# Kernel optimization log

Hardware: AMD Instinct MI355X
Metric: run time of the kernel (lower is better)

## Reference

```python
import jax, jax.numpy as jnp
import numpy as np

N, E, DIN, DH, DC = 50000, 1600000, 128, 128, 40
EPS = 1e-5  # BatchNorm eps


def _seg_sum(v, idx, n):
    return jax.ops.segment_sum(v, idx, num_segments=n)


def setup_inputs() -> dict:
    key = jax.random.key(0)
    ks = jax.random.split(key, 24)
    rn = lambda i, shp, s=0.05: jax.random.normal(ks[i], shp, jnp.float32) * s
    return {
        "x": jax.random.normal(ks[0], (N, DIN), jnp.float32),
        "src": jax.random.randint(ks[1], (E,), 0, N, jnp.int32),
        "dst": jax.random.randint(ks[2], (E,), 0, N, jnp.int32),
        # CoNet layer 1 (in -> hidden)
        "w11s": rn(3, (DIN, DH)), "w11n": rn(4, (DIN, DH)), "b11": jnp.zeros((DH,), jnp.float32),
        "w12": rn(5, (DIN, DH)), "b12": jnp.zeros((DH,), jnp.float32),
        "w13": rn(6, (DIN, DH)), "a13l": rn(7, (DH,)), "a13r": rn(8, (DH,)), "b13": jnp.zeros((DH,), jnp.float32),
        "cw1": jax.random.uniform(ks[9], (3,), jnp.float32, 0.5, 1.5),
        # BatchNorm1d
        "g": jnp.ones((DH,), jnp.float32), "be": jnp.zeros((DH,), jnp.float32),
        # CoNet layer 2 (hidden -> out)
        "w21s": rn(10, (DH, DC)), "w21n": rn(11, (DH, DC)), "b21": jnp.zeros((DC,), jnp.float32),
        "w22": rn(12, (DH, DC)), "b22": jnp.zeros((DC,), jnp.float32),
        "w23": rn(13, (DH, DC)), "a23l": rn(14, (DC,)), "a23r": rn(15, (DC,)), "b23": jnp.zeros((DC,), jnp.float32),
        "cw2": jax.random.uniform(ks[16], (3,), jnp.float32, 0.5, 1.5),
    }


def conet(x, src, dst, ws, wn, bs, wg, bg, wa, al, ar, ba, cw):
    """AFFN CoNet: SAGE(mean) + GCN + GAT(1 head), fused by normalized weights."""
    n = x.shape[0]
    ones = jnp.ones((src.shape[0],), x.dtype)
    indeg = _seg_sum(ones, dst, n)   # in-degree per node
    outdeg = _seg_sum(ones, src, n)  # out-degree per node

    # --- SAGEConv, mean aggregator: fc_self(x) + fc_neigh(mean_neigh(x)) ---
    nei = _seg_sum(x[src], dst, n) / jnp.maximum(indeg, 1.0)[:, None]
    x1 = x @ ws + nei @ wn + bs

    ns = jnp.maximum(outdeg, 1.0) ** -0.5
    nd = jnp.maximum(indeg, 1.0) ** -0.5
    h = _seg_sum((x * ns[:, None])[src], dst, n) * nd[:, None]
    x2 = h @ wg + bg

    # --- GATConv, 1 head ---
    f = x @ wa                       # [N, out]
    el = f @ al                      # [N]
    er = f @ ar                      # [N]
    e = jax.nn.leaky_relu(el[src] + er[dst], 0.2)  # [E]
    m = jax.ops.segment_max(e, dst, num_segments=n)
    a = jnp.exp(e - m[dst])
    s = _seg_sum(a, dst, n)
    alpha = a / jnp.maximum(s[dst], 1e-9)
    x3 = _seg_sum(alpha[:, None] * f[src], dst, n) + ba

    w = cw / jnp.sum(cw)
    return w[0] * x1 + w[1] * x2 + w[2] * x3


def reference(x, src, dst,
              w11s, w11n, b11, w12, b12, w13, a13l, a13r, b13, cw1,
              g, be,
              w21s, w21n, b21, w22, b22, w23, a23l, a23r, b23, cw2):
    h = conet(x, src, dst, w11s, w11n, b11, w12, b12, w13, a13l, a13r, b13, cw1)
    # BatchNorm1d (training-mode batch statistics)
    mu = jnp.mean(h, axis=0)
    var = jnp.var(h, axis=0)
    h = (h - mu) * jax.lax.rsqrt(var + EPS) * g + be
    h = jax.nn.relu(h)
    # dropout in eval mode: identity
    h = conet(h, src, dst, w21s, w21n, b21, w22, b22, w23, a23l, a23r, b23, cw2)
    return jax.nn.log_softmax(h, axis=1)
```

## Files before the change

### kernel.cpp

```cpp
#include <hip/hip_runtime.h>
#include <hip/hip_bf16.h>
#include <math.h>

#define DIN 128
#define DH  128
#define DC  40

#define HCHUNK  12544
#define NSTRIPE 128
#define NPAD    (HCHUNK * 4)

typedef unsigned short u16;
typedef unsigned int u32;
typedef unsigned char u8;
typedef __attribute__((ext_vector_type(2))) float f32x2;
typedef __attribute__((ext_vector_type(4))) float f32x4;
typedef __attribute__((ext_vector_type(8))) short bf16x8;

static __device__ __forceinline__ float bf2f(u16 u) {
    union { u32 i; float f; } v; v.i = ((u32)u) << 16; return v.f;
}
static __device__ __forceinline__ u16 f2bf(float f) {
    __hip_bfloat16 h = __float2bfloat16(f);
    union { __hip_bfloat16 h; u16 u; } v; v.h = h; return v.u;
}
static __device__ __forceinline__ u32 pack2bf(float a, float b) {
    return ((u32)f2bf(b) << 16) | (u32)f2bf(a);
}

static __device__ __forceinline__ u8 f2fp8(float f) {
    u32 s = (__float_as_uint(f) >> 31) << 7;
    float a = fabsf(f);
    a = fminf(a, 448.f);
    if (a < 0.015625f) {
        int q = (int)rintf(a * 512.f);
        return (u8)(s | (u32)q);
    }
    u32 x = __float_as_uint(a);
    u32 lsb = (x >> 20) & 1;
    x += 0x0007FFFF + lsb;
    u32 e = (x >> 23) - 120;
    u32 m = (x >> 20) & 7;
    return (u8)(s | (e << 3) | m);
}

#if __has_builtin(__builtin_amdgcn_cvt_pk_f32_fp8)
template<bool HI>
static __device__ __forceinline__ f32x2 fp8pk(u32 w) {
    return __builtin_amdgcn_cvt_pk_f32_fp8((int)w, HI);
}
#else
static __device__ __forceinline__ float fp8dec1(u32 byte) {
    u32 s = (byte >> 7) & 1, em = byte & 0x7F;
    float v = __uint_as_float((s << 31) | (em << 20)) * 0x1p120f;
    return v;
}
template<bool HI>
static __device__ __forceinline__ f32x2 fp8pk(u32 w) {
    u32 b0 = HI ? ((w >> 16) & 0xff) : (w & 0xff);
    u32 b1 = HI ? ((w >> 24) & 0xff) : ((w >> 8) & 0xff);
    f32x2 r; r.x = fp8dec1(b0); r.y = fp8dec1(b1); return r;
}
#endif

__global__ __launch_bounds__(256) void k_prep(
        const float* w11s, const float* w11n, const float* w12, const float* w13,
        const float* b11, const float* b12, const float* b13, const float* cw1,
        const float* w21s, const float* w21n, const float* w22, const float* w23,
        const float* b21, const float* b22, const float* b23, const float* cw2,
        const float* a13l, const float* a13r, const float* a23l, const float* a23r,
        u16* __restrict__ Wf1, u16* __restrict__ Wf2,
        float* __restrict__ bc1, float* __restrict__ bc2, float* __restrict__ vattn) {
    int i = blockIdx.x * 256 + threadIdx.x;
    float s1 = cw1[0] + cw1[1] + cw1[2];
    float u0 = cw1[0] / s1, u1 = cw1[1] / s1, u2 = cw1[2] / s1;
    float s2 = cw2[0] + cw2[1] + cw2[2];
    float q0 = cw2[0] / s2, q1 = cw2[1] / s2, q2 = cw2[2] / s2;
    if (i < 65536) {
        int j = i & 7, lane = (i >> 3) & 63, nt = (i >> 9) & 7, kt = i >> 12;
        int k = kt * 32 + ((lane >> 4) << 3) + j;
        int n = nt * 16 + (lane & 15);
        float v;
        if (k < 128)      v = u0 * w11s[k * 128 + n];
        else if (k < 256) v = u0 * w11n[(k - 128) * 128 + n];
        else if (k < 384) v = u1 * w12[(k - 256) * 128 + n];
        else              v = u2 * w13[(k - 384) * 128 + n];
        Wf1[i] = f2bf(v);
    } else if (i < 90112) {
        int i2 = i - 65536;
        int j = i2 & 7;
        int l2 = i2 >> 3;
        int lane = l2 & 63;
        int t2 = l2 >> 6;
        int nt = t2 % 3, kt = t2 / 3;
        int k = kt * 32 + ((lane >> 4) << 3) + j;
        int n = nt * 16 + (lane & 15);
        float v = 0.f;
        if (n < 40) {
            if (k < 128)      v = q0 * w21s[k * 40 + n];
            else if (k < 256) v = q0 * w21n[(k - 128) * 40 + n];
            else if (k < 384) v = q1 * w22[(k - 256) * 40 + n];
            else              v = q2 * w23[(k - 384) * 40 + n];
        }
        Wf2[i2] = f2bf(v);
    } else if (i < 90624) {
        int t = i - 90112;
        if (t < 128) {
            float s = 0; for (int j = 0; j < 128; ++j) s += w13[t * 128 + j] * a13l[j];
            vattn[t] = s;
        } else if (t < 256) {
            int r = t - 128; float s = 0; for (int j = 0; j < 128; ++j) s += w13[r * 128 + j] * a13r[j];
            vattn[t] = s;
        } else if (t < 384) {
            int r = t - 256; float s = 0; for (int j = 0; j < 40; ++j) s += w23[r * 40 + j] * a23l[j];
            vattn[t] = s;
        } else {
            int r = t - 384; float s = 0; for (int j = 0; j < 40; ++j) s += w23[r * 40 + j] * a23r[j];
            vattn[t] = s;
        }
    } else if (i < 90752) {
        int c = i - 90624;
        bc1[c] = u0 * b11[c] + u1 * b12[c] + u2 * b13[c];
    } else if (i < 90792) {
        int c = i - 90752;
        bc2[c] = q0 * b21[c] + q1 * b22[c] + q2 * b23[c];
    }
}

__global__ __launch_bounds__(256) void k_hist2(const int* __restrict__ src,
        const int* __restrict__ dst,
        u16* __restrict__ partialsS, u16* __restrict__ partialsD,
        u16* __restrict__ wsrank, int E, int eps) {
    __shared__ u32 histS[HCHUNK];
    __shared__ u32 histD[HCHUNK];
    int chunk = blockIdx.x;
    int stripe = blockIdx.y;
    int base = chunk * (HCHUNK * 2);
    for (int i = threadIdx.x; i < HCHUNK; i += 256) { histS[i] = 0; histD[i] = 0; }
    __syncthreads();
    int e0 = stripe * eps;
    int e1 = e0 + eps; if (e1 > E) e1 = E;
    for (int e = e0 + threadIdx.x; e < e1; e += 256) {
        int ks = src[e] - base;
        int kd = dst[e] - base;
        if ((u32)ks < (u32)(HCHUNK * 2))
            atomicAdd(&histS[ks >> 1], 1u << ((ks & 1) * 16));
        if ((u32)kd < (u32)(HCHUNK * 2)) {
            u32 old = atomicAdd(&histD[kd >> 1], 1u << ((kd & 1) * 16));
            wsrank[e] = (u16)((old >> ((kd & 1) * 16)) & 0xffff);
        }
    }
    __syncthreads();
    u32* prowS = (u32*)(partialsS + (size_t)stripe * NPAD + base);
    u32* prowD = (u32*)(partialsD + (size_t)stripe * NPAD + base);
    for (int i = threadIdx.x; i < HCHUNK; i += 256) { prowS[i] = histS[i]; prowD[i] = histD[i]; }
}

__global__ void k_pfx2(const u16* __restrict__ partialsS, u16* __restrict__ partialsD,
                       int* __restrict__ indeg, float* __restrict__ ns, int n) {
    int node = blockIdx.x * 256 + threadIdx.x;
    if (node >= NPAD) return;
    int runS = 0;
    for (int s0 = 0; s0 < NSTRIPE; s0 += 16) {
        u16 c[16];
#pragma unroll
        for (int i = 0; i < 16; ++i) c[i] = partialsS[(size_t)(s0 + i) * NPAD + node];
#pragma unroll
        for (int i = 0; i < 16; ++i) runS += c[i];
    }
    int runD = 0;
    for (int s0 = 0; s0 < NSTRIPE; s0 += 16) {
        u16 c[16];
#pragma unroll
        for (int i = 0; i < 16; ++i) c[i] = partialsD[(size_t)(s0 + i) * NPAD + node];
#pragma unroll
        for (int i = 0; i < 16; ++i) {
            partialsD[(size_t)(s0 + i) * NPAD + node] = (u16)runD;
            runD += c[i];
        }
    }
    if (node < n) {
        indeg[node] = runD;
        int d = runS < 1 ? 1 : runS;
        ns[node] = rsqrtf((float)d);
    }
}

__global__ void k_scan1(const int* __restrict__ deg, int* __restrict__ excl,
                        int* __restrict__ bsum, int n) {
    __shared__ int sh[256];
    int i = blockIdx.x * 256 + threadIdx.x;
    int v = (i < n) ? deg[i] : 0;
    sh[threadIdx.x] = v; __syncthreads();
    for (int o = 1; o < 256; o <<= 1) {
        int t = (threadIdx.x >= o) ? sh[threadIdx.x - o] : 0;
        __syncthreads(); sh[threadIdx.x] += t; __syncthreads();
    }
    if (i < n) excl[i] = sh[threadIdx.x] - v;
    if (threadIdx.x == 255) bsum[blockIdx.x] = sh[255];
}
__global__ void k_scan2(int* __restrict__ bsum, int nb) {
    __shared__ int sh[256];
    int t = threadIdx.x;
    int v = (t < nb) ? bsum[t] : 0;
    sh[t] = v; __syncthreads();
    for (int o = 1; o < 256; o <<= 1) {
        int u = (t >= o) ? sh[t - o] : 0;
        __syncthreads(); sh[t] += u; __syncthreads();
    }
    if (t < nb) bsum[t] = sh[t] - v;
}
__global__ void k_scan3(const int* __restrict__ excl, const int* __restrict__ bsum,
                        int* __restrict__ rowptr, int n, int E) {
    int i = blockIdx.x * 256 + threadIdx.x;
    if (i < n) rowptr[i] = excl[i] + bsum[blockIdx.x];
    if (i == 0) rowptr[n] = E;
}

__global__ __launch_bounds__(256) void k_place2(const int* __restrict__ src,
        const int* __restrict__ dst, const int* __restrict__ rowptr,
        const u16* __restrict__ partials, const u16* __restrict__ wsrank,
        int* __restrict__ col, int E, int eps) {
    int stripe = blockIdx.x;
    const u16* prow = partials + (size_t)stripe * NPAD;
    int sub = (eps + 3) >> 2;
    int e0 = stripe * eps + blockIdx.y * sub;
    int e1 = e0 + sub;
    int cap = stripe * eps + eps; if (cap > E) cap = E;
    if (e1 > cap) e1 = cap;
    for (int e = e0 + threadIdx.x; e < e1; e += 256) {
        int d = dst[e];
        col[rowptr[d] + prow[d] + wsrank[e]] = src[e];
    }
}

__global__ __launch_bounds__(256) void k_cvt_dots(const float* __restrict__ X,
        const float* __restrict__ vl, const float* __restrict__ vr, const float* __restrict__ ns,
        u16* __restrict__ Xb, u8* __restrict__ Xq,
        float2* __restrict__ elns, float* __restrict__ er, int n) {
    int w = (blockIdx.x * blockDim.x + threadIdx.x) >> 6;
    int lane = threadIdx.x & 63;
    if (w >= n) return;
    float2 xv = *(const float2*)&X[(size_t)w * 128 + lane * 2];
    *(u32*)&Xb[(size_t)w * 128 + lane * 2] = pack2bf(xv.x, xv.y);
    u16 q = (u16)f2fp8(xv.x) | ((u16)f2fp8(xv.y) << 8);
    *(u16*)&Xq[(size_t)w * 128 + lane * 2] = q;
    float2 a = *(const float2*)&vl[lane * 2];
    float2 b = *(const float2*)&vr[lane * 2];
    float dl = xv.x * a.x + xv.y * a.y;
    float dr = xv.x * b.x + xv.y * b.y;
    for (int off = 32; off; off >>= 1) {
        dl += __shfl_down(dl, off);
        dr += __shfl_down(dr, off);
    }
    if (lane == 0) { elns[w] = make_float2(dl, ns[w]); er[w] = dr; }
}

__global__ __launch_bounds__(256) void k_agg(const u8* __restrict__ Xq,
        const int* __restrict__ rowptr, const int* __restrict__ colsrc,
        const float2* __restrict__ elns, const float* __restrict__ er,
        u16* __restrict__ AG, int n) {
    int w = (blockIdx.x * blockDim.x + threadIdx.x) >> 6;
    int lane = threadIdx.x & 63;
    if (w >= n) return;
    int g = lane >> 4, gl = lane & 15;
    int beg = rowptr[w], end = rowptr[w + 1];
    int k = end - beg;
    float erd = er[w];
    f32x2 aS2[4] = {}, aG2[4] = {}, aA2[4] = {};
    float ssum = 0.f;
    for (int c0 = beg; c0 < end; c0 += 64) {
        int cnt = end - c0; if (cnt > 64) cnt = 64;
        int s = 0; float p = 0.f; float nsl = 0.f;
        if (lane < cnt) {
            s = colsrc[c0 + lane];
            float2 v = elns[s];
            float t = v.x + erd;
            t = t > 0.f ? t : 0.2f * t;
            p = __expf(t);
            nsl = v.y;
        }
        float ps = p;
        for (int o = 32; o; o >>= 1) ps += __shfl_xor(ps, o);
        ssum += ps;
        int full = cnt >> 2;
#pragma unroll 8
        for (int t = 0; t < full; ++t) {
            int j = (t << 2) + g;
            int sj = __shfl(s, j);
            float pj = __shfl(p, j);
            float nsj = __shfl(nsl, j);
            uint2 xq = *(const uint2*)&Xq[(size_t)sj * 128 + gl * 8];
            f32x2 xv2[4] = {fp8pk<false>(xq.x), fp8pk<true>(xq.x),
                            fp8pk<false>(xq.y), fp8pk<true>(xq.y)};
            f32x2 ns2 = {nsj, nsj}, p2 = {pj, pj};
#pragma unroll
            for (int q = 0; q < 4; ++q) {
                aS2[q] += xv2[q];
                aG2[q] += ns2 * xv2[q];
                aA2[q] += p2 * xv2[q];
            }
        }
        if (cnt & 3) {
            int j = (full << 2) + g;
            int sj = __shfl(s, j);
            float pj = __shfl(p, j);
            float nsj = __shfl(nsl, j);
            if (j < cnt) {
                uint2 xq = *(const uint2*)&Xq[(size_t)sj * 128 + gl * 8];
                f32x2 xv2[4] = {fp8pk<false>(xq.x), fp8pk<true>(xq.x),
                                fp8pk<false>(xq.y), fp8pk<true>(xq.y)};
                f32x2 ns2 = {nsj, nsj}, p2 = {pj, pj};
#pragma unroll
                for (int q = 0; q < 4; ++q) {
                    aS2[q] += xv2[q];
                    aG2[q] += ns2 * xv2[q];
                    aA2[q] += p2 * xv2[q];
                }
            }
        }
    }
    float aS[8], aG[8], aA[8];
#pragma unroll
    for (int i = 0; i < 4; ++i) {
        aS[2 * i] = aS2[i][0]; aS[2 * i + 1] = aS2[i][1];
        aG[2 * i] = aG2[i][0]; aG[2 * i + 1] = aG2[i][1];
        aA[2 * i] = aA2[i][0]; aA[2 * i + 1] = aA2[i][1];
    }
#pragma unroll
    for (int i = 0; i < 8; ++i) {
        aS[i] += __shfl_xor(aS[i], 16); aS[i] += __shfl_xor(aS[i], 32);
        aG[i] += __shfl_xor(aG[i], 16); aG[i] += __shfl_xor(aG[i], 32);
        aA[i] += __shfl_xor(aA[i], 16); aA[i] += __shfl_xor(aA[i], 32);
    }
    int kc = k < 1 ? 1 : k;
    float invk = 1.f / (float)kc;
    float ndd = rsqrtf((float)kc);
    float gi = 1.f / fmaxf(ssum, 1e-9f);
    u16* row = AG + (size_t)w * 384;
    if (g == 0) {
        uint4 o = make_uint4(pack2bf(aS[0] * invk, aS[1] * invk), pack2bf(aS[2] * invk, aS[3] * invk),
                             pack2bf(aS[4] * invk, aS[5] * invk), pack2bf(aS[6] * invk, aS[7] * invk));
        *(uint4*)&row[gl * 8] = o;
    } else if (g == 1) {
        uint4 o = make_uint4(pack2bf(aG[0] * ndd, aG[1] * ndd), pack2bf(aG[2] * ndd, aG[3] * ndd),
                             pack2bf(aG[4] * ndd, aG[5] * ndd), pack2bf(aG[6] * ndd, aG[7] * ndd));
        *(uint4*)&row[128 + gl * 8] = o;
    } else if (g == 2) {
        uint4 o = make_uint4(pack2bf(aA[0] * gi, aA[1] * gi), pack2bf(aA[2] * gi, aA[3] * gi),
                             pack2bf(aA[4] * gi, aA[5] * gi), pack2bf(aA[6] * gi, aA[7] * gi));
        *(uint4*)&row[256 + gl * 8] = o;
    }
}

__global__ __launch_bounds__(256) void k_gemm1(const u16* __restrict__ Xb,
        const u16* __restrict__ AG, const u16* __restrict__ Wf,
        const float* __restrict__ bias, u16* __restrict__ C,
        float* __restrict__ bnacc, int M) {
    if (blockIdx.x == 0 && threadIdx.x < 256) bnacc[threadIdx.x] = 0.f;
    const int NT = 8;
    int wave = threadIdx.x >> 6;
    int lane = threadIdx.x & 63;
    int m0 = blockIdx.x * 64 + wave * 16;
    int arow = m0 + (lane & 15);
    if (arow >= M) arow = M - 1;
    int kq = lane >> 4;
    f32x4 acc[NT];
#pragma unroll
    for (int t = 0; t < NT; ++t) acc[t] = (f32x4){0.f, 0.f, 0.f, 0.f};
#pragma unroll
    for (int kt = 0; kt < 16; ++kt) {
        int k0 = kt * 32 + kq * 8;
        bf16x8 a;
        if (k0 < 128) a = *(const bf16x8*)&Xb[(size_t)arow * 128 + k0];
        else          a = *(const bf16x8*)&AG[(size_t)arow * 384 + (k0 - 128)];
        const u16* wb = Wf + ((size_t)kt * NT) * 512 + lane * 8;
#pragma unroll
        for (int t = 0; t < NT; ++t) {
            bf16x8 b = *(const bf16x8*)&wb[(size_t)t * 512];
            acc[t] = __builtin_amdgcn_mfma_f32_16x16x32_bf16(a, b, acc[t], 0, 0, 0);
        }
    }
    int ccol = lane & 15;
    int rbase = m0 + kq * 4;
#pragma unroll
    for (int t = 0; t < NT; ++t) {
        int col = t * 16 + ccol;
        float bv = bias[col];
#pragma unroll
        for (int r = 0; r < 4; ++r) {
            int rr = rbase + r;
            if (rr < M) C[(size_t)rr * 128 + col] = f2bf(acc[t][r] + bv);
        }
    }
}

__global__ __launch_bounds__(256) void k_gemm2_lsm(const u16* __restrict__ Xb,
        const u16* __restrict__ AG, const u16* __restrict__ Wf,
        const float* __restrict__ bias, float* __restrict__ out, int M) {
    const int NT = 3;
    int wave = threadIdx.x >> 6;
    int lane = threadIdx.x & 63;
    int m0 = blockIdx.x * 64 + wave * 16;
    int arow = m0 + (lane & 15);
    if (arow >= M) arow = M - 1;
    int kq = lane >> 4;
    f32x4 acc[NT];
#pragma unroll
    for (int t = 0; t < NT; ++t) acc[t] = (f32x4){0.f, 0.f, 0.f, 0.f};
#pragma unroll
    for (int kt = 0; kt < 16; ++kt) {
        int k0 = kt * 32 + kq * 8;
        bf16x8 a;
        if (k0 < 128) a = *(const bf16x8*)&Xb[(size_t)arow * 128 + k0];
        else          a = *(const bf16x8*)&AG[(size_t)arow * 384 + (k0 - 128)];
        const u16* wb = Wf + ((size_t)kt * NT) * 512 + lane * 8;
#pragma unroll
        for (int t = 0; t < NT; ++t) {
            bf16x8 b = *(const bf16x8*)&wb[(size_t)t * 512];
            acc[t] = __builtin_amdgcn_mfma_f32_16x16x32_bf16(a, b, acc[t], 0, 0, 0);
        }
    }
    int ccol = lane & 15;
    int rbase = m0 + kq * 4;
    bool valid[NT];
    float bv[NT];
#pragma unroll
    for (int t = 0; t < NT; ++t) {
        int col = t * 16 + ccol;
        valid[t] = (col < 40);
        bv[t] = valid[t] ? bias[col] : 0.f;
    }
#pragma unroll
    for (int r = 0; r < 4; ++r) {
        float v[NT];
#pragma unroll
        for (int t = 0; t < NT; ++t) v[t] = valid[t] ? (acc[t][r] + bv[t]) : -INFINITY;
        float mx = fmaxf(fmaxf(v[0], v[1]), v[2]);
        for (int o = 1; o < 16; o <<= 1) mx = fmaxf(mx, __shfl_xor(mx, o));
        float se = 0.f;
#pragma unroll
        for (int t = 0; t < NT; ++t) se += valid[t] ? __expf(v[t] - mx) : 0.f;
        for (int o = 1; o < 16; o <<= 1) se += __shfl_xor(se, o);
        float lse = mx + logf(se);
        int rr = rbase + r;
        if (rr < M) {
#pragma unroll
            for (int t = 0; t < NT; ++t) {
                int col = t * 16 + ccol;
                if (valid[t]) out[(size_t)rr * 40 + col] = v[t] - lse;
            }
        }
    }
}

__global__ __launch_bounds__(256) void k_bn_stats(const u16* __restrict__ H,
        float* __restrict__ acc, int nrows) {
    int c = threadIdx.x & 127;
    int rh = threadIdx.x >> 7;
    int r0 = blockIdx.x * 256;
    int rend = r0 + 256; if (rend > nrows) rend = nrows;
    float s = 0.f, q = 0.f;
    for (int r = r0 + rh; r < rend; r += 2) {
        float v = bf2f(H[(size_t)r * 128 + c]);
        s += v; q += v * v;
    }
    atomicAdd(&acc[c], s);
    atomicAdd(&acc[128 + c], q);
}

__global__ __launch_bounds__(256) void k_bnorm_dots(const u16* __restrict__ Hp,
        const float* __restrict__ bnacc, const float* __restrict__ g, const float* __restrict__ be,
        const float* __restrict__ vl, const float* __restrict__ vr,
        const float* __restrict__ ns,
        u16* __restrict__ H, u8* __restrict__ H8,
        float2* __restrict__ elns, float* __restrict__ er, float Nf, int n) {
    int w = (blockIdx.x * blockDim.x + threadIdx.x) >> 6;
    int lane = threadIdx.x & 63;
    if (w >= n) return;
    int c0 = lane * 2, c1 = lane * 2 + 1;
    float mu0 = bnacc[c0] / Nf, mu1 = bnacc[c1] / Nf;
    float var0 = bnacc[128 + c0] / Nf - mu0 * mu0;
    float var1 = bnacc[128 + c1] / Nf - mu1 * mu1;
    float sc0 = g[c0] * rsqrtf(var0 + 1e-5f);
    float sc1 = g[c1] * rsqrtf(var1 + 1e-5f);
    float sh0 = be[c0] - mu0 * sc0;
    float sh1 = be[c1] - mu1 * sc1;
    u32 hu = *(const u32*)&Hp[(size_t)w * 128 + lane * 2];
    float vx = bf2f((u16)hu), vy = bf2f((u16)(hu >> 16));
    float h0 = fmaxf(vx * sc0 + sh0, 0.f);
    float h1 = fmaxf(vy * sc1 + sh1, 0.f);
    *(u32*)&H[(size_t)w * 128 + lane * 2] = pack2bf(h0, h1);
    u16 q = (u16)f2fp8(h0) | ((u16)f2fp8(h1) << 8);
    *(u16*)&H8[(size_t)w * 128 + lane * 2] = q;
    float2 a = *(const float2*)&vl[lane * 2];
    float2 b = *(const float2*)&vr[lane * 2];
    float dl = h0 * a.x + h1 * a.y;
    float dr = h0 * b.x + h1 * b.y;
    for (int off = 32; off; off >>= 1) {
        dl += __shfl_down(dl, off);
        dr += __shfl_down(dr, off);
    }
    if (lane == 0) { elns[w] = make_float2(dl, ns[w]); er[w] = dr; }
}

extern "C" void kernel_launch(void* const* d_in, const int* in_sizes, int n_in,
                              void* d_out, int out_size, void* d_ws, size_t ws_size,
                              hipStream_t stream) {
    const float* x    = (const float*)d_in[0];
    const int*   src  = (const int*)d_in[1];
    const int*   dst  = (const int*)d_in[2];
    const float* w11s = (const float*)d_in[3];
    const float* w11n = (const float*)d_in[4];
    const float* b11  = (const float*)d_in[5];
    const float* w12  = (const float*)d_in[6];
    const float* b12  = (const float*)d_in[7];
    const float* w13  = (const float*)d_in[8];
    const float* a13l = (const float*)d_in[9];
    const float* a13r = (const float*)d_in[10];
    const float* b13  = (const float*)d_in[11];
    const float* cw1  = (const float*)d_in[12];
    const float* g    = (const float*)d_in[13];
    const float* be   = (const float*)d_in[14];
    const float* w21s = (const float*)d_in[15];
    const float* w21n = (const float*)d_in[16];
    const float* b21  = (const float*)d_in[17];
    const float* w22  = (const float*)d_in[18];
    const float* b22  = (const float*)d_in[19];
    const float* w23  = (const float*)d_in[20];
    const float* a23l = (const float*)d_in[21];
    const float* a23r = (const float*)d_in[22];
    const float* b23  = (const float*)d_in[23];
    const float* cw2  = (const float*)d_in[24];

    const int N = in_sizes[0] / DIN;
    const int E = in_sizes[1];

    char* ws = (char*)d_ws;
    size_t off = 0;
    auto alloc = [&](size_t bytes) { size_t o = off; off += (bytes + 255) & ~(size_t)255; return o; };
    u16*   Xb     = (u16*)(ws + alloc((size_t)N * 128 * 2));
    u8*    Xq     = (u8*)(ws + alloc((size_t)N * 128));
    u16*   AG     = (u16*)(ws + alloc((size_t)N * 384 * 2));
    u16*   hpre   = (u16*)(ws + alloc((size_t)N * 128 * 2));
    u16*   h      = (u16*)(ws + alloc((size_t)N * 128 * 2));
    u8*    h8     = (u8*)(ws + alloc((size_t)N * 128));
    int*   col    = (int*)(ws + alloc((size_t)E * 4));
    u16*   wsrank = (u16*)(ws + alloc((size_t)E * 2));
    u16*   partialsS = (u16*)(ws + alloc((size_t)NSTRIPE * NPAD * 2));
    u16*   partialsD = (u16*)(ws + alloc((size_t)NSTRIPE * NPAD * 2));
    int*   rowptr = (int*)(ws + alloc((size_t)(N + 1) * 4));
    int*   indeg  = (int*)(ws + alloc((size_t)N * 4));
    int*   excl   = (int*)(ws + alloc((size_t)N * 4));
    int*   bsum   = (int*)(ws + alloc(256 * 4));
    float* ns     = (float*)(ws + alloc((size_t)N * 4));
    float2* elns  = (float2*)(ws + alloc((size_t)N * 8));
    float* er     = (float*)(ws + alloc((size_t)N * 4));
    u16*   Wf1    = (u16*)(ws + alloc((size_t)16 * 8 * 64 * 8 * 2));
    u16*   Wf2    = (u16*)(ws + alloc((size_t)16 * 3 * 64 * 8 * 2));
    float* bc1    = (float*)(ws + alloc(128 * 4));
    float* bc2    = (float*)(ws + alloc(40 * 4));
    float* vattn  = (float*)(ws + alloc(512 * 4));
    float* bnacc  = (float*)(ws + alloc(256 * 4));

    int eb_eps = (E + NSTRIPE - 1) / NSTRIPE;
    int wb = (N * 64 + 255) / 256;
    int sb = (N + 255) / 256;
    int gb = (N + 63) / 64;
    int pb = (NPAD + 255) / 256;

    k_prep<<<(90792 + 255) / 256, 256, 0, stream>>>(
        w11s, w11n, w12, w13, b11, b12, b13, cw1,
        w21s, w21n, w22, w23, b21, b22, b23, cw2,
        a13l, a13r, a23l, a23r, Wf1, Wf2, bc1, bc2, vattn);

    {
        dim3 hg(2, NSTRIPE);
        k_hist2<<<hg, 256, 0, stream>>>(src, dst, partialsS, partialsD, wsrank, E, eb_eps);
        k_pfx2<<<pb, 256, 0, stream>>>(partialsS, partialsD, indeg, ns, N);
        k_scan1<<<sb, 256, 0, stream>>>(indeg, excl, bsum, N);
        k_scan2<<<1, 256, 0, stream>>>(bsum, sb);
        k_scan3<<<sb, 256, 0, stream>>>(excl, bsum, rowptr, N, E);
        dim3 pg(NSTRIPE, 4);
        k_place2<<<pg, 256, 0, stream>>>(src, dst, rowptr, partialsD, wsrank, col, E, eb_eps);
    }

    k_cvt_dots<<<wb, 256, 0, stream>>>(x, vattn, vattn + 128, ns, Xb, Xq, elns, er, N);
    k_agg<<<wb, 256, 0, stream>>>(Xq, rowptr, col, elns, er, AG, N);
    k_gemm1<<<gb, 256, 0, stream>>>(Xb, AG, Wf1, bc1, hpre, bnacc, N);

    k_bn_stats<<<(N + 255) / 256, 256, 0, stream>>>(hpre, bnacc, N);
    k_bnorm_dots<<<wb, 256, 0, stream>>>(hpre, bnacc, g, be, vattn + 256, vattn + 384, ns,
                                         h, h8, elns, er, (float)N, N);

    k_agg<<<wb, 256, 0, stream>>>(h8, rowptr, col, elns, er, AG, N);
    k_gemm2_lsm<<<gb, 256, 0, stream>>>(h, AG, Wf2, bc2, (float*)d_out, N);
}
```

Before: 426.1 us.

## Build CSR with global atomic counting and cursors; pad aggregation tails

Replaces the striped shared-memory histogram, per-stripe prefix and rank-based placement with two simple edge-parallel kernels. One counts in- and out-degrees with global atomics, the other places edges with an atomicAdd on a per-node cursor. This drops the large partials buffers and their reads and writes. The out-degree normalisation is now computed inside the conversion and batchnorm kernels, and the degree arrays and a zero padding row are cleared in the prep kernel. The aggregation loop pads partial groups with a zero sentinel node so the separate tail branch goes away. The trade-offs are atomic contention, a nondeterministic neighbour order and summation order, and extra zero-weight gathers in the padded groups.

```diff
diff --git a/kernel.cpp b/kernel.cpp
--- a/kernel.cpp
+++ b/kernel.cpp
@@ -5,10 +5,6 @@
 #define DIN 128
 #define DH  128
 #define DC  40
-
-#define HCHUNK  12544
-#define NSTRIPE 128
-#define NPAD    (HCHUNK * 4)
 
 typedef unsigned short u16;
 typedef unsigned int u32;
@@ -70,7 +66,9 @@
         const float* b21, const float* b22, const float* b23, const float* cw2,
         const float* a13l, const float* a13r, const float* a23l, const float* a23r,
         u16* __restrict__ Wf1, u16* __restrict__ Wf2,
-        float* __restrict__ bc1, float* __restrict__ bc2, float* __restrict__ vattn) {
+        float* __restrict__ bc1, float* __restrict__ bc2, float* __restrict__ vattn,
+        int* __restrict__ indeg, int* __restrict__ outdeg,
+        u32* __restrict__ zq, u32* __restrict__ zh, int n) {
     int i = blockIdx.x * 256 + threadIdx.x;
     float s1 = cw1[0] + cw1[1] + cw1[2];
     float u0 = cw1[0] / s1, u1 = cw1[1] / s1, u2 = cw1[2] / s1;
@@ -79,12 +77,12 @@
     if (i < 65536) {
         int j = i & 7, lane = (i >> 3) & 63, nt = (i >> 9) & 7, kt = i >> 12;
         int k = kt * 32 + ((lane >> 4) << 3) + j;
-        int n = nt * 16 + (lane & 15);
+        int n2 = nt * 16 + (lane & 15);
         float v;
-        if (k < 128)      v = u0 * w11s[k * 128 + n];
-        else if (k < 256) v = u0 * w11n[(k - 128) * 128 + n];
-        else if (k < 384) v = u1 * w12[(k - 256) * 128 + n];
-        else              v = u2 * w13[(k - 384) * 128 + n];
+        if (k < 128)      v = u0 * w11s[k * 128 + n2];
+        else if (k < 256) v = u0 * w11n[(k - 128) * 128 + n2];
+        else if (k < 384) v = u1 * w12[(k - 256) * 128 + n2];
+        else              v = u2 * w13[(k - 384) * 128 + n2];
         Wf1[i] = f2bf(v);
     } else if (i < 90112) {
         int i2 = i - 65536;
@@ -94,13 +92,13 @@
         int t2 = l2 >> 6;
         int nt = t2 % 3, kt = t2 / 3;
         int k = kt * 32 + ((lane >> 4) << 3) + j;
-        int n = nt * 16 + (lane & 15);
+        int n2 = nt * 16 + (lane & 15);
         float v = 0.f;
-        if (n < 40) {
-            if (k < 128)      v = q0 * w21s[k * 40 + n];
-            else if (k < 256) v = q0 * w21n[(k - 128) * 40 + n];
-            else if (k < 384) v = q1 * w22[(k - 256) * 40 + n];
-            else              v = q2 * w23[(k - 384) * 40 + n];
+        if (n2 < 40) {
+            if (k < 128)      v = q0 * w21s[k * 40 + n2];
+            else if (k < 256) v = q0 * w21n[(k - 128) * 40 + n2];
+            else if (k < 384) v = q1 * w22[(k - 256) * 40 + n2];
+            else              v = q2 * w23[(k - 384) * 40 + n2];
         }
         Wf2[i2] = f2bf(v);
     } else if (i < 90624) {
@@ -124,65 +122,22 @@
     } else if (i < 90792) {
         int c = i - 90752;
         bc2[c] = q0 * b21[c] + q1 * b22[c] + q2 * b23[c];
-    }
-}
-
-__global__ __launch_bounds__(256) void k_hist2(const int* __restrict__ src,
-        const int* __restrict__ dst,
-        u16* __restrict__ partialsS, u16* __restrict__ partialsD,
-        u16* __restrict__ wsrank, int E, int eps) {
-    __shared__ u32 histS[HCHUNK];
-    __shared__ u32 histD[HCHUNK];
-    int chunk = blockIdx.x;
-    int stripe = blockIdx.y;
-    int base = chunk * (HCHUNK * 2);
-    for (int i = threadIdx.x; i < HCHUNK; i += 256) { histS[i] = 0; histD[i] = 0; }
-    __syncthreads();
-    int e0 = stripe * eps;
-    int e1 = e0 + eps; if (e1 > E) e1 = E;
-    for (int e = e0 + threadIdx.x; e < e1; e += 256) {
-        int ks = src[e] - base;
-        int kd = dst[e] - base;
-        if ((u32)ks < (u32)(HCHUNK * 2))
-            atomicAdd(&histS[ks >> 1], 1u << ((ks & 1) * 16));
-        if ((u32)kd < (u32)(HCHUNK * 2)) {
-            u32 old = atomicAdd(&histD[kd >> 1], 1u << ((kd & 1) * 16));
-            wsrank[e] = (u16)((old >> ((kd & 1) * 16)) & 0xffff);
-        }
-    }
-    __syncthreads();
-    u32* prowS = (u32*)(partialsS + (size_t)stripe * NPAD + base);
-    u32* prowD = (u32*)(partialsD + (size_t)stripe * NPAD + base);
-    for (int i = threadIdx.x; i < HCHUNK; i += 256) { prowS[i] = histS[i]; prowD[i] = histD[i]; }
-}
-
-__global__ void k_pfx2(const u16* __restrict__ partialsS, u16* __restrict__ partialsD,
-                       int* __restrict__ indeg, float* __restrict__ ns, int n) {
-    int node = blockIdx.x * 256 + threadIdx.x;
-    if (node >= NPAD) return;
-    int runS = 0;
-    for (int s0 = 0; s0 < NSTRIPE; s0 += 16) {
-        u16 c[16];
-#pragma unroll
-        for (int i = 0; i < 16; ++i) c[i] = partialsS[(size_t)(s0 + i) * NPAD + node];
-#pragma unroll
-        for (int i = 0; i < 16; ++i) runS += c[i];
-    }
-    int runD = 0;
-    for (int s0 = 0; s0 < NSTRIPE; s0 += 16) {
-        u16 c[16];
-#pragma unroll
-        for (int i = 0; i < 16; ++i) c[i] = partialsD[(size_t)(s0 + i) * NPAD + node];
-#pragma unroll
-        for (int i = 0; i < 16; ++i) {
-            partialsD[(size_t)(s0 + i) * NPAD + node] = (u16)runD;
-            runD += c[i];
-        }
-    }
-    if (node < n) {
-        indeg[node] = runD;
-        int d = runS < 1 ? 1 : runS;
-        ns[node] = rsqrtf((float)d);
+    } else if (i < 90792 + 2 * n) {
+        int t = i - 90792;
+        if (t < n) indeg[t] = 0; else outdeg[t - n] = 0;
+    } else if (i < 90792 + 2 * n + 64) {
+        int t = i - 90792 - 2 * n;
+        if (t < 32) zq[t] = 0u; else zh[t - 32] = 0u;
+    }
+}
+
+__global__ __launch_bounds__(256) void k_count(const int* __restrict__ src,
+        const int* __restrict__ dst, int* __restrict__ indeg,
+        int* __restrict__ outdeg, int E) {
+    int i = blockIdx.x * 256 + threadIdx.x;
+    if (i < E) {
+        atomicAdd(&indeg[dst[i]], 1);
+        atomicAdd(&outdeg[src[i]], 1);
     }
 }
 
@@ -211,31 +166,29 @@
     if (t < nb) bsum[t] = sh[t] - v;
 }
 __global__ void k_scan3(const int* __restrict__ excl, const int* __restrict__ bsum,
-                        int* __restrict__ rowptr, int n, int E) {
+                        int* __restrict__ rowptr, int* __restrict__ cursor, int n, int E) {
     int i = blockIdx.x * 256 + threadIdx.x;
-    if (i < n) rowptr[i] = excl[i] + bsum[blockIdx.x];
+    if (i < n) {
+        int v = excl[i] + bsum[blockIdx.x];
+        rowptr[i] = v;
+        cursor[i] = v;
+    }
     if (i == 0) rowptr[n] = E;
 }
 
-__global__ __launch_bounds__(256) void k_place2(const int* __restrict__ src,
-        const int* __restrict__ dst, const int* __restrict__ rowptr,
-        const u16* __restrict__ partials, const u16* __restrict__ wsrank,
-        int* __restrict__ col, int E, int eps) {
-    int stripe = blockIdx.x;
-    const u16* prow = partials + (size_t)stripe * NPAD;
-    int sub = (eps + 3) >> 2;
-    int e0 = stripe * eps + blockIdx.y * sub;
-    int e1 = e0 + sub;
-    int cap = stripe * eps + eps; if (cap > E) cap = E;
-    if (e1 > cap) e1 = cap;
-    for (int e = e0 + threadIdx.x; e < e1; e += 256) {
-        int d = dst[e];
-        col[rowptr[d] + prow[d] + wsrank[e]] = src[e];
+__global__ __launch_bounds__(256) void k_place(const int* __restrict__ src,
+        const int* __restrict__ dst, int* __restrict__ cursor,
+        int* __restrict__ col, int E) {
+    int i = blockIdx.x * 256 + threadIdx.x;
+    if (i < E) {
+        int pos = atomicAdd(&cursor[dst[i]], 1);
+        col[pos] = src[i];
     }
 }
 
 __global__ __launch_bounds__(256) void k_cvt_dots(const float* __restrict__ X,
-        const float* __restrict__ vl, const float* __restrict__ vr, const float* __restrict__ ns,
+        const float* __restrict__ vl, const float* __restrict__ vr,
+        const int* __restrict__ odeg,
         u16* __restrict__ Xb, u8* __restrict__ Xq,
         float2* __restrict__ elns, float* __restrict__ er, int n) {
     int w = (blockIdx.x * blockDim.x + threadIdx.x) >> 6;
@@ -253,7 +206,12 @@
         dl += __shfl_down(dl, off);
         dr += __shfl_down(dr, off);
     }
-    if (lane == 0) { elns[w] = make_float2(dl, ns[w]); er[w] = dr; }
+    if (lane == 0) {
+        int od = odeg[w];
+        float nsw = rsqrtf((float)(od < 1 ? 1 : od));
+        elns[w] = make_float2(dl, nsw);
+        er[w] = dr;
+    }
 }
 
 __global__ __launch_bounds__(256) void k_agg(const u8* __restrict__ Xq,
@@ -271,7 +229,7 @@
     float ssum = 0.f;
     for (int c0 = beg; c0 < end; c0 += 64) {
         int cnt = end - c0; if (cnt > 64) cnt = 64;
-        int s = 0; float p = 0.f; float nsl = 0.f;
+        int s = n; float p = 0.f; float nsl = 0.f;
         if (lane < cnt) {
             s = colsrc[c0 + lane];
             float2 v = elns[s];
@@ -283,9 +241,9 @@
         float ps = p;
         for (int o = 32; o; o >>= 1) ps += __shfl_xor(ps, o);
         ssum += ps;
-        int full = cnt >> 2;
+        int steps = (cnt + 3) >> 2;
 #pragma unroll 8
-        for (int t = 0; t < full; ++t) {
+        for (int t = 0; t < steps; ++t) {
             int j = (t << 2) + g;
             int sj = __shfl(s, j);
             float pj = __shfl(p, j);
@@ -299,24 +257,6 @@
                 aS2[q] += xv2[q];
                 aG2[q] += ns2 * xv2[q];
                 aA2[q] += p2 * xv2[q];
-            }
-        }
-        if (cnt & 3) {
-            int j = (full << 2) + g;
-            int sj = __shfl(s, j);
-            float pj = __shfl(p, j);
-            float nsj = __shfl(nsl, j);
-            if (j < cnt) {
-                uint2 xq = *(const uint2*)&Xq[(size_t)sj * 128 + gl * 8];
-                f32x2 xv2[4] = {fp8pk<false>(xq.x), fp8pk<true>(xq.x),
-                                fp8pk<false>(xq.y), fp8pk<true>(xq.y)};
-                f32x2 ns2 = {nsj, nsj}, p2 = {pj, pj};
-#pragma unroll
-                for (int q = 0; q < 4; ++q) {
-                    aS2[q] += xv2[q];
-                    aG2[q] += ns2 * xv2[q];
-                    aA2[q] += p2 * xv2[q];
-                }
             }
         }
     }
@@ -472,7 +412,7 @@
 __global__ __launch_bounds__(256) void k_bnorm_dots(const u16* __restrict__ Hp,
         const float* __restrict__ bnacc, const float* __restrict__ g, const float* __restrict__ be,
         const float* __restrict__ vl, const float* __restrict__ vr,
-        const float* __restrict__ ns,
+        const int* __restrict__ odeg,
         u16* __restrict__ H, u8* __restrict__ H8,
         float2* __restrict__ elns, float* __restrict__ er, float Nf, int n) {
     int w = (blockIdx.x * blockDim.x + threadIdx.x) >> 6;
@@ -501,7 +441,12 @@
         dl += __shfl_down(dl, off);
         dr += __shfl_down(dr, off);
     }
-    if (lane == 0) { elns[w] = make_float2(dl, ns[w]); er[w] = dr; }
+    if (lane == 0) {
+        int od = odeg[w];
+        float nsw = rsqrtf((float)(od < 1 ? 1 : od));
+        elns[w] = make_float2(dl, nsw);
+        er[w] = dr;
+    }
 }
 
 extern "C" void kernel_launch(void* const* d_in, const int* in_sizes, int n_in,
@@ -540,20 +485,18 @@
     size_t off = 0;
     auto alloc = [&](size_t bytes) { size_t o = off; off += (bytes + 255) & ~(size_t)255; return o; };
     u16*   Xb     = (u16*)(ws + alloc((size_t)N * 128 * 2));
-    u8*    Xq     = (u8*)(ws + alloc((size_t)N * 128));
+    u8*    Xq     = (u8*)(ws + alloc((size_t)(N + 1) * 128));
     u16*   AG     = (u16*)(ws + alloc((size_t)N * 384 * 2));
     u16*   hpre   = (u16*)(ws + alloc((size_t)N * 128 * 2));
     u16*   h      = (u16*)(ws + alloc((size_t)N * 128 * 2));
-    u8*    h8     = (u8*)(ws + alloc((size_t)N * 128));
+    u8*    h8     = (u8*)(ws + alloc((size_t)(N + 1) * 128));
     int*   col    = (int*)(ws + alloc((size_t)E * 4));
-    u16*   wsrank = (u16*)(ws + alloc((size_t)E * 2));
-    u16*   partialsS = (u16*)(ws + alloc((size_t)NSTRIPE * NPAD * 2));
-    u16*   partialsD = (u16*)(ws + alloc((size_t)NSTRIPE * NPAD * 2));
     int*   rowptr = (int*)(ws + alloc((size_t)(N + 1) * 4));
     int*   indeg  = (int*)(ws + alloc((size_t)N * 4));
+    int*   outdeg = (int*)(ws + alloc((size_t)N * 4));
+    int*   cursor = (int*)(ws + alloc((size_t)N * 4));
     int*   excl   = (int*)(ws + alloc((size_t)N * 4));
     int*   bsum   = (int*)(ws + alloc(256 * 4));
-    float* ns     = (float*)(ws + alloc((size_t)N * 4));
     float2* elns  = (float2*)(ws + alloc((size_t)N * 8));
     float* er     = (float*)(ws + alloc((size_t)N * 4));
     u16*   Wf1    = (u16*)(ws + alloc((size_t)16 * 8 * 64 * 8 * 2));
@@ -563,34 +506,30 @@
     float* vattn  = (float*)(ws + alloc(512 * 4));
     float* bnacc  = (float*)(ws + alloc(256 * 4));
 
-    int eb_eps = (E + NSTRIPE - 1) / NSTRIPE;
     int wb = (N * 64 + 255) / 256;
     int sb = (N + 255) / 256;
     int gb = (N + 63) / 64;
-    int pb = (NPAD + 255) / 256;
-
-    k_prep<<<(90792 + 255) / 256, 256, 0, stream>>>(
+    int eb = (E + 255) / 256;
+    int prep_total = 90792 + 2 * N + 64;
+
+    k_prep<<<(prep_total + 255) / 256, 256, 0, stream>>>(
         w11s, w11n, w12, w13, b11, b12, b13, cw1,
         w21s, w21n, w22, w23, b21, b22, b23, cw2,
-        a13l, a13r, a23l, a23r, Wf1, Wf2, bc1, bc2, vattn);
-
-    {
-        dim3 hg(2, NSTRIPE);
-        k_hist2<<<hg, 256, 0, stream>>>(src, dst, partialsS, partialsD, wsrank, E, eb_eps);
-        k_pfx2<<<pb, 256, 0, stream>>>(partialsS, partialsD, indeg, ns, N);
-        k_scan1<<<sb, 256, 0, stream>>>(indeg, excl, bsum, N);
-        k_scan2<<<1, 256, 0, stream>>>(bsum, sb);
-        k_scan3<<<sb, 256, 0, stream>>>(excl, bsum, rowptr, N, E);
-        dim3 pg(NSTRIPE, 4);
-        k_place2<<<pg, 256, 0, stream>>>(src, dst, rowptr, partialsD, wsrank, col, E, eb_eps);
-    }
-
-    k_cvt_dots<<<wb, 256, 0, stream>>>(x, vattn, vattn + 128, ns, Xb, Xq, elns, er, N);
+        a13l, a13r, a23l, a23r, Wf1, Wf2, bc1, bc2, vattn,
+        indeg, outdeg, (u32*)(Xq + (size_t)N * 128), (u32*)(h8 + (size_t)N * 128), N);
+
+    k_count<<<eb, 256, 0, stream>>>(src, dst, indeg, outdeg, E);
+    k_scan1<<<sb, 256, 0, stream>>>(indeg, excl, bsum, N);
+    k_scan2<<<1, 256, 0, stream>>>(bsum, sb);
+    k_scan3<<<sb, 256, 0, stream>>>(excl, bsum, rowptr, cursor, N, E);
+    k_place<<<eb, 256, 0, stream>>>(src, dst, cursor, col, E);
+
+    k_cvt_dots<<<wb, 256, 0, stream>>>(x, vattn, vattn + 128, outdeg, Xb, Xq, elns, er, N);
     k_agg<<<wb, 256, 0, stream>>>(Xq, rowptr, col, elns, er, AG, N);
     k_gemm1<<<gb, 256, 0, stream>>>(Xb, AG, Wf1, bc1, hpre, bnacc, N);
 
     k_bn_stats<<<(N + 255) / 256, 256, 0, stream>>>(hpre, bnacc, N);
-    k_bnorm_dots<<<wb, 256, 0, stream>>>(hpre, bnacc, g, be, vattn + 256, vattn + 384, ns,
+    k_bnorm_dots<<<wb, 256, 0, stream>>>(hpre, bnacc, g, be, vattn + 256, vattn + 384, outdeg,
                                          h, h8, elns, er, (float)N, N);
 
     k_agg<<<wb, 256, 0, stream>>>(h8, rowptr, col, elns, er, AG, N);
```

Result: slower. 615.6 us (+44.5%).
